# Optimization experiments

Measured on AMD Instinct MI355X. Metric: run time of the kernel, lower is better.

The kernel has to match this reference:

```python
import jax, jax.numpy as jnp
import numpy as np

N_HEAD = 16
ROPE_THETA = 10000.0


def rope_cos_sin(head_dim, T):
    # theta_i = 1 / ROPE_THETA**(2i/d), freqs = outer(positions, theta)
    inv_freq = 1.0 / (ROPE_THETA ** (np.arange(0, head_dim, 2, dtype=np.float32) / head_dim))
    pos = np.arange(T, dtype=np.float32)
    freqs = np.outer(pos, inv_freq)  # [T, d/2]
    return jnp.asarray(np.cos(freqs)), jnp.asarray(np.sin(freqs))


def apply_rope(x, cos, sin):
    # x: [B, T, H, d]; pairs are consecutive lanes (..., d/2, 2) like view_as_complex
    B, T, H, d = x.shape
    xp = x.reshape(B, T, H, d // 2, 2)
    x0, x1 = xp[..., 0], xp[..., 1]
    c = cos[None, :, None, :]  # [1, T, 1, d/2]
    s = sin[None, :, None, :]
    r0 = x0 * c - x1 * s
    r1 = x0 * s + x1 * c
    return jnp.stack([r0, r1], axis=-1).reshape(B, T, H, d)


def setup_inputs() -> dict:
    key = jax.random.key(0)
    k1, k2, k3 = jax.random.split(key, 3)
    B, T, C = 2, 2048, 1024
    x = jax.random.normal(k1, (B, T, C), dtype=jnp.float32)
    w_qkv = jax.random.normal(k2, (C, 3 * C), dtype=jnp.float32) * (1.0 / np.sqrt(C))
    w_proj = jax.random.normal(k3, (C, C), dtype=jnp.float32) * (1.0 / np.sqrt(C))
    b_proj = jnp.zeros((C,), dtype=jnp.float32)
    return {"x": x, "w_qkv": w_qkv, "w_proj": w_proj, "b_proj": b_proj}


def reference(x, w_qkv, w_proj, b_proj):
    B, T, C = x.shape
    H = N_HEAD
    d = C // H
    qkv = x @ w_qkv  # [B, T, 3C]
    q, k, v = jnp.split(qkv, 3, axis=-1)
    q = q.reshape(B, T, H, d)
    k = k.reshape(B, T, H, d)
    v = v.reshape(B, T, H, d)
    cos, sin = rope_cos_sin(d, T)
    q = apply_rope(q, cos, sin)
    k = apply_rope(k, cos, sin)
    # causal SDPA
    scale = 1.0 / np.sqrt(d).astype(np.float32)
    scores = jnp.einsum('bqhd,bkhd->bhqk', q, k) * scale  # [B, H, T, T]
    causal = jnp.tril(jnp.ones((T, T), dtype=bool))
    scores = jnp.where(causal[None, None], scores, jnp.finfo(scores.dtype).min)
    attn = jax.nn.softmax(scores, axis=-1)
    y = jnp.einsum('bhqk,bkhd->bqhd', attn, v).reshape(B, T, C)
    return y @ w_proj + b_proj
```

## Files before the change

kernel.cpp:

```cpp
#include <hip/hip_runtime.h>
#include <hip/hip_bf16.h>
#include <math.h>

typedef __bf16 bf16x8 __attribute__((ext_vector_type(8)));
typedef float floatx4 __attribute__((ext_vector_type(4)));

#define BM 128
#define BN 128

__device__ __forceinline__ void load_lds16(const void* g, void* l) {
    __builtin_amdgcn_global_load_lds(
        (const __attribute__((address_space(1))) void*)g,
        (__attribute__((address_space(3))) void*)l, 16, 0, 0);
}

__global__ __launch_bounds__(256)
void cvt_bf16_kernel(const float* __restrict__ in, __hip_bfloat16* __restrict__ out, int n8)
{
    int i = (blockIdx.x * 256 + threadIdx.x);
    if (i >= n8) return;
    const float4 a = *reinterpret_cast<const float4*>(in + (size_t)i * 8);
    const float4 b = *reinterpret_cast<const float4*>(in + (size_t)i * 8 + 4);
    union { __hip_bfloat162 h[4]; uint4 u; } pk;
    pk.h[0] = __float22bfloat162_rn(make_float2(a.x, a.y));
    pk.h[1] = __float22bfloat162_rn(make_float2(a.z, a.w));
    pk.h[2] = __float22bfloat162_rn(make_float2(b.x, b.y));
    pk.h[3] = __float22bfloat162_rn(make_float2(b.z, b.w));
    *reinterpret_cast<uint4*>(out + (size_t)i * 8) = pk.u;
}

__global__ __launch_bounds__(256)
void transpose_cvt_kernel(const float* __restrict__ in, __hip_bfloat16* __restrict__ out,
                          int R, int C)
{
    __shared__ float Ts[64][68];
    const int c0 = blockIdx.x * 64;
    const int r0 = blockIdx.y * 64;
    const int t  = threadIdx.x;
    const int lr = t >> 2;
    const int lc = (t & 3) * 16;
    #pragma unroll
    for (int j = 0; j < 16; j += 4) {
        float4 v = *reinterpret_cast<const float4*>(in + (size_t)(r0 + lr) * C + c0 + lc + j);
        Ts[lr][lc + j + 0] = v.x;
        Ts[lr][lc + j + 1] = v.y;
        Ts[lr][lc + j + 2] = v.z;
        Ts[lr][lc + j + 3] = v.w;
    }
    __syncthreads();
    const int oc = t >> 2;
    const int rs = (t & 3) * 16;
    __hip_bfloat16 tmp[16];
    #pragma unroll
    for (int j = 0; j < 16; ++j)
        tmp[j] = __float2bfloat16(Ts[rs + j][oc]);
    __hip_bfloat16* op = out + (size_t)(c0 + oc) * R + r0 + rs;
    *reinterpret_cast<uint4*>(op)     = *reinterpret_cast<uint4*>(tmp);
    *reinterpret_cast<uint4*>(op + 8) = *reinterpret_cast<uint4*>(tmp + 8);
}

template<int EPI, int CONV, int BKT, int M, int N, int K>
__global__ __launch_bounds__(256)
void gemm_kernel(const void* __restrict__ Avoid,
                 const void* __restrict__ Bvoid,
                 const float* __restrict__ bias,
                 __hip_bfloat16* __restrict__ Qo,
                 __hip_bfloat16* __restrict__ Ko,
                 __hip_bfloat16* __restrict__ Vt,
                 float* __restrict__ Out)
{
    constexpr int LD = (CONV == 0) ? BKT : 40;
    __shared__ __align__(16) __hip_bfloat16 As[BM][LD];
    __shared__ __align__(16) __hip_bfloat16 Bs[BN][LD];

    const int t    = threadIdx.x;
    const int m0   = blockIdx.y * BM;
    const int n0   = blockIdx.x * BN;
    const int lane = t & 63;
    const int w    = t >> 6;
    const int wm   = (w >> 1) * 64;
    const int wn   = (w & 1) * 64;
    const int quad = lane >> 4;
    const int l16  = lane & 15;

    floatx4 acc[4][4] = {};

    if (CONV == 0 && BKT == 32) {
        const __hip_bfloat16* A  = (const __hip_bfloat16*)Avoid;
        const __hip_bfloat16* Bt = (const __hip_bfloat16*)Bvoid;
        const int r16 = lane >> 2;
        const int gor = (lane & 3) ^ ((lane >> 3) & 3);
        const int sg  = (quad ^ ((l16 >> 1) & 3)) * 8;

        for (int k0 = 0; k0 < K; k0 += 32) {
            #pragma unroll
            for (int i = 0; i < 2; ++i) {
                int c   = 2 * w + i;
                int row = c * 16 + r16;
                load_lds16(A  + (size_t)(m0 + row) * K + k0 + gor * 8, &As[c * 16][0]);
                load_lds16(Bt + (size_t)(n0 + row) * K + k0 + gor * 8, &Bs[c * 16][0]);
            }
            __syncthreads();
            bf16x8 af[4], bfr[4];
            #pragma unroll
            for (int mf = 0; mf < 4; ++mf)
                af[mf] = *reinterpret_cast<const bf16x8*>(&As[wm + mf * 16 + l16][sg]);
            #pragma unroll
            for (int nf = 0; nf < 4; ++nf)
                bfr[nf] = *reinterpret_cast<const bf16x8*>(&Bs[wn + nf * 16 + l16][sg]);
            #pragma unroll
            for (int mf = 0; mf < 4; ++mf)
                #pragma unroll
                for (int nf = 0; nf < 4; ++nf)
                    acc[mf][nf] = __builtin_amdgcn_mfma_f32_16x16x32_bf16(
                        af[mf], bfr[nf], acc[mf][nf], 0, 0, 0);
            __syncthreads();
        }
    } else if (CONV == 0) {
        const __hip_bfloat16* A  = (const __hip_bfloat16*)Avoid;
        const __hip_bfloat16* Bt = (const __hip_bfloat16*)Bvoid;
        const int drow = lane >> 3;
        const int gsrc = (lane & 7) ^ drow;
        const int xk   = l16 & 7;

        for (int k0 = 0; k0 < K; k0 += 64) {
            #pragma unroll
            for (int i = 0; i < 4; ++i) {
                int c   = 4 * w + i;
                int row = c * 8 + drow;
                load_lds16(A  + (size_t)(m0 + row) * K + k0 + gsrc * 8, &As[c * 8][0]);
                load_lds16(Bt + (size_t)(n0 + row) * K + k0 + gsrc * 8, &Bs[c * 8][0]);
            }
            __syncthreads();
            #pragma unroll
            for (int kb = 0; kb < 2; ++kb) {
                bf16x8 af[4], bfr[4];
                #pragma unroll
                for (int mf = 0; mf < 4; ++mf)
                    af[mf] = *reinterpret_cast<const bf16x8*>(
                        &As[wm + mf * 16 + l16][((kb * 4 + quad) ^ xk) * 8]);
                #pragma unroll
                for (int nf = 0; nf < 4; ++nf)
                    bfr[nf] = *reinterpret_cast<const bf16x8*>(
                        &Bs[wn + nf * 16 + l16][((kb * 4 + quad) ^ xk) * 8]);
                #pragma unroll
                for (int mf = 0; mf < 4; ++mf)
                    #pragma unroll
                    for (int nf = 0; nf < 4; ++nf)
                        acc[mf][nf] = __builtin_amdgcn_mfma_f32_16x16x32_bf16(
                            af[mf], bfr[nf], acc[mf][nf], 0, 0, 0);
            }
            __syncthreads();
        }
    } else {
        const int sg = quad * 8;
        for (int k0 = 0; k0 < K; k0 += 32) {
            if (EPI == 0) {
                const float* A = (const float*)Avoid;
                #pragma unroll
                for (int i = 0; i < 4; ++i) {
                    int slot = t + i * 256;
                    int row  = slot >> 3;
                    int c4   = (slot & 7) << 2;
                    float4 v = *reinterpret_cast<const float4*>(A + (size_t)(m0 + row) * K + k0 + c4);
                    union { __hip_bfloat162 h2[2]; uint2 u; } pk;
                    pk.h2[0] = __float22bfloat162_rn(make_float2(v.x, v.y));
                    pk.h2[1] = __float22bfloat162_rn(make_float2(v.z, v.w));
                    *reinterpret_cast<uint2*>(&As[row][c4]) = pk.u;
                }
            } else {
                const __hip_bfloat16* A = (const __hip_bfloat16*)Avoid;
                #pragma unroll
                for (int i = 0; i < 2; ++i) {
                    int idx = t + i * 256;
                    int row = idx >> 2;
                    int col = (idx & 3) << 3;
                    *reinterpret_cast<uint4*>(&As[row][col]) =
                        *reinterpret_cast<const uint4*>(A + (size_t)(m0 + row) * K + k0 + col);
                }
            }
            const float* B = (const float*)Bvoid;
            const int bn  = t & 127;
            const int bkh = (t >> 7) * 16;
            float f[16];
            #pragma unroll
            for (int j = 0; j < 16; ++j)
                f[j] = B[(size_t)(k0 + bkh + j) * N + n0 + bn];
            #pragma unroll
            for (int c = 0; c < 4; ++c) {
                union { __hip_bfloat162 h2[2]; uint2 u; } pk;
                pk.h2[0] = __float22bfloat162_rn(make_float2(f[4*c + 0], f[4*c + 1]));
                pk.h2[1] = __float22bfloat162_rn(make_float2(f[4*c + 2], f[4*c + 3]));
                *reinterpret_cast<uint2*>(&Bs[bn][bkh + 4*c]) = pk.u;
            }
            __syncthreads();

            bf16x8 af[4], bfr[4];
            #pragma unroll
            for (int mf = 0; mf < 4; ++mf)
                af[mf] = *reinterpret_cast<const bf16x8*>(&As[wm + mf * 16 + l16][sg]);
            #pragma unroll
            for (int nf = 0; nf < 4; ++nf)
                bfr[nf] = *reinterpret_cast<const bf16x8*>(&Bs[wn + nf * 16 + l16][sg]);
            #pragma unroll
            for (int mf = 0; mf < 4; ++mf)
                #pragma unroll
                for (int nf = 0; nf < 4; ++nf)
                    acc[mf][nf] = __builtin_amdgcn_mfma_f32_16x16x32_bf16(
                        af[mf], bfr[nf], acc[mf][nf], 0, 0, 0);
            __syncthreads();
        }
    }

    if (EPI == 0) {
        #pragma unroll
        for (int mf = 0; mf < 4; ++mf) {
            #pragma unroll
            for (int nf = 0; nf < 4; ++nf) {
                #pragma unroll
                for (int r = 0; r < 4; ++r) {
                    float v = acc[mf][nf][r];
                    int m  = m0 + wm + mf * 16 + quad * 4 + r;
                    int n  = n0 + wn + nf * 16 + l16;
                    int bb = m >> 11;
                    int tp = m & 2047;
                    int which = n >> 10;
                    int dd = n & 63;
                    int h  = (n & 1023) >> 6;
                    float other = __shfl_xor(v, 1);
                    if (which < 2) {
                        int f = dd >> 1;
                        float inv = exp2f((float)f * -0.4152410118609203f);
                        float ang = (float)tp * inv;
                        float s, c;
                        __sincosf(ang, &s, &c);
                        v = (dd & 1) ? (other * s + v * c) : (v * c - other * s);
                        if (which == 0) v *= 0.1803368801111137f;
                    }
                    __hip_bfloat16 bv = __float2bfloat16(v);
                    size_t bh = (size_t)bb * 16 + h;
                    if (which == 0)      Qo[(bh * 2048 + tp) * 64 + dd] = bv;
                    else if (which == 1) Ko[(bh * 2048 + tp) * 64 + dd] = bv;
                    else                 Vt[(bh * 64 + dd) * 2048 + tp] = bv;
                }
            }
        }
    } else {
        #pragma unroll
        for (int mf = 0; mf < 4; ++mf)
            #pragma unroll
            for (int nf = 0; nf < 4; ++nf)
                #pragma unroll
                for (int r = 0; r < 4; ++r) {
                    int m = m0 + wm + mf * 16 + quad * 4 + r;
                    int n = n0 + wn + nf * 16 + l16;
                    Out[(size_t)m * N + n] = acc[mf][nf][r] + bias[n];
                }
    }
}

__global__ __launch_bounds__(256)
void attn_kernel(const __hip_bfloat16* __restrict__ Q,
                 const __hip_bfloat16* __restrict__ Kb,
                 const __hip_bfloat16* __restrict__ Vt,
                 __hip_bfloat16* __restrict__ Y)
{
    const int bh = blockIdx.x;
    const int qt = 31 - (int)blockIdx.y;
    const int bb = bh >> 4;
    const int h  = bh & 15;
    const int t    = threadIdx.x;
    const int w    = t >> 6;
    const int lane = t & 63;
    const int quad = lane >> 4;
    const int l16  = lane & 15;
    const int T = 2048;

    __shared__ __align__(16) __hip_bfloat16 Ks[64][72];
    __shared__ __align__(16) __hip_bfloat16 Vs[64][72];
    __shared__ __align__(16) __hip_bfloat16 Pl[4][16][72];

    const __hip_bfloat16* Qp = Q  + (size_t)bh * T * 64;
    const __hip_bfloat16* Kp = Kb + (size_t)bh * T * 64;
    const __hip_bfloat16* Vp = Vt + (size_t)bh * 64 * T;

    const int qrow0 = qt * 64 + w * 16;

    bf16x8 qa[2];
    #pragma unroll
    for (int kb = 0; kb < 2; ++kb)
        qa[kb] = *reinterpret_cast<const bf16x8*>(
            Qp + (size_t)(qrow0 + l16) * 64 + kb * 32 + quad * 8);

    bf16x8 ones;
    #pragma unroll
    for (int j = 0; j < 8; ++j) ones[j] = (__bf16)1.0f;

    floatx4 o[4] = {};
    floatx4 sums = {};

    const int srow = t >> 2;
    const int sch  = t & 3;
    const int ntiles = qt + 1;

    bf16x8 kreg[2], vreg[2];
    {
        const __hip_bfloat16* kg = Kp + (size_t)srow * 64 + sch * 8;
        kreg[0] = *reinterpret_cast<const bf16x8*>(kg);
        kreg[1] = *reinterpret_cast<const bf16x8*>(kg + 32);
        const __hip_bfloat16* vg = Vp + (size_t)srow * T + sch * 8;
        vreg[0] = *reinterpret_cast<const bf16x8*>(vg);
        vreg[1] = *reinterpret_cast<const bf16x8*>(vg + 32);
    }

    for (int kt = 0; kt < ntiles; ++kt) {
        __syncthreads();
        *reinterpret_cast<bf16x8*>(&Ks[srow][sch * 8])      = kreg[0];
        *reinterpret_cast<bf16x8*>(&Ks[srow][sch * 8 + 32]) = kreg[1];
        *reinterpret_cast<bf16x8*>(&Vs[srow][sch * 8])      = vreg[0];
        *reinterpret_cast<bf16x8*>(&Vs[srow][sch * 8 + 32]) = vreg[1];
        __syncthreads();
        if (kt + 1 < ntiles) {
            const __hip_bfloat16* kg = Kp + (size_t)((kt + 1) * 64 + srow) * 64 + sch * 8;
            kreg[0] = *reinterpret_cast<const bf16x8*>(kg);
            kreg[1] = *reinterpret_cast<const bf16x8*>(kg + 32);
            const __hip_bfloat16* vg = Vp + (size_t)srow * T + (kt + 1) * 64 + sch * 8;
            vreg[0] = *reinterpret_cast<const bf16x8*>(vg);
            vreg[1] = *reinterpret_cast<const bf16x8*>(vg + 32);
        }

        floatx4 sfr[4];
        #pragma unroll
        for (int nf = 0; nf < 4; ++nf) {
            floatx4 s = {};
            #pragma unroll
            for (int kb = 0; kb < 2; ++kb) {
                bf16x8 kf = *reinterpret_cast<const bf16x8*>(&Ks[nf * 16 + l16][kb * 32 + quad * 8]);
                s = __builtin_amdgcn_mfma_f32_16x16x32_bf16(qa[kb], kf, s, 0, 0, 0);
            }
            sfr[nf] = s;
        }
        if (kt == qt) {
            #pragma unroll
            for (int nf = 0; nf < 4; ++nf)
                #pragma unroll
                for (int r = 0; r < 4; ++r) {
                    int qg = w * 16 + quad * 4 + r;
                    int kg = nf * 16 + l16;
                    if (kg > qg) sfr[nf][r] = -INFINITY;
                }
        }
        #pragma unroll
        for (int nf = 0; nf < 4; ++nf)
            #pragma unroll
            for (int r = 0; r < 4; ++r)
                Pl[w][quad * 4 + r][nf * 16 + l16] = __float2bfloat16(exp2f(sfr[nf][r]));
        bf16x8 pa[2];
        #pragma unroll
        for (int kb = 0; kb < 2; ++kb)
            pa[kb] = *reinterpret_cast<const bf16x8*>(&Pl[w][l16][kb * 32 + quad * 8]);

        sums = __builtin_amdgcn_mfma_f32_16x16x32_bf16(pa[0], ones, sums, 0, 0, 0);
        sums = __builtin_amdgcn_mfma_f32_16x16x32_bf16(pa[1], ones, sums, 0, 0, 0);

        #pragma unroll
        for (int nf = 0; nf < 4; ++nf) {
            #pragma unroll
            for (int kb = 0; kb < 2; ++kb) {
                bf16x8 vb = *reinterpret_cast<const bf16x8*>(&Vs[nf * 16 + l16][kb * 32 + quad * 8]);
                o[nf] = __builtin_amdgcn_mfma_f32_16x16x32_bf16(pa[kb], vb, o[nf], 0, 0, 0);
            }
        }
    }

    #pragma unroll
    for (int r = 0; r < 4; ++r) {
        float inv = 1.0f / sums[r];
        #pragma unroll
        for (int nf = 0; nf < 4; ++nf) {
            float v = o[nf][r] * inv;
            int qrow = qrow0 + quad * 4 + r;
            int dd = nf * 16 + l16;
            Y[((size_t)bb * 2048 + qrow) * 1024 + h * 64 + dd] = __float2bfloat16(v);
        }
    }
}

extern "C" void kernel_launch(void* const* d_in, const int* in_sizes, int n_in,
                              void* d_out, int out_size, void* d_ws, size_t ws_size,
                              hipStream_t stream) {
    const float* x      = (const float*)d_in[0];
    const float* w_qkv  = (const float*)d_in[1];
    const float* w_proj = (const float*)d_in[2];
    const float* b_proj = (const float*)d_in[3];
    float* out = (float*)d_out;

    const size_t NELT = (size_t)4096 * 1024;
    const size_t WQKV = (size_t)3072 * 1024;
    const size_t WPRJ = (size_t)1024 * 1024;
    const size_t need_main = (4 * NELT + WQKV + WPRJ) * 2;
    const size_t need_fb   = 3 * NELT * 2;

    dim3 blk(256);

    if (ws_size >= need_main) {
        __hip_bfloat16* Q      = (__hip_bfloat16*)d_ws;
        __hip_bfloat16* Kb     = Q   + NELT;
        __hip_bfloat16* Vt     = Kb  + NELT;
        __hip_bfloat16* xb     = Vt  + NELT;
        __hip_bfloat16* wqkvT  = xb  + NELT;
        __hip_bfloat16* wprjT  = wqkvT + WQKV;

        cvt_bf16_kernel<<<dim3((NELT / 8 + 255) / 256), blk, 0, stream>>>(x, xb, NELT / 8);
        transpose_cvt_kernel<<<dim3(3072 / 64, 1024 / 64), blk, 0, stream>>>(w_qkv, wqkvT, 1024, 3072);
        transpose_cvt_kernel<<<dim3(1024 / 64, 1024 / 64), blk, 0, stream>>>(w_proj, wprjT, 1024, 1024);

        gemm_kernel<0, 0, 32, 4096, 3072, 1024><<<dim3(24, 32), blk, 0, stream>>>(
            xb, wqkvT, nullptr, Q, Kb, Vt, nullptr);
        attn_kernel<<<dim3(32, 32), blk, 0, stream>>>(Q, Kb, Vt, xb);
        gemm_kernel<1, 0, 64, 4096, 1024, 1024><<<dim3(8, 32), blk, 0, stream>>>(
            xb, wprjT, b_proj, nullptr, nullptr, nullptr, out);
    } else if (ws_size >= need_fb) {
        __hip_bfloat16* Q  = (__hip_bfloat16*)d_ws;
        __hip_bfloat16* Kb = Q  + NELT;
        __hip_bfloat16* Vt = Kb + NELT;

        gemm_kernel<0, 1, 32, 4096, 3072, 1024><<<dim3(24, 32), blk, 0, stream>>>(
            x, w_qkv, nullptr, Q, Kb, Vt, nullptr);
        attn_kernel<<<dim3(32, 32), blk, 0, stream>>>(Q, Kb, Vt, (__hip_bfloat16*)d_out);
        hipMemcpyAsync(Q, d_out, NELT * sizeof(__hip_bfloat16), hipMemcpyDeviceToDevice, stream);
        gemm_kernel<1, 1, 32, 4096, 1024, 1024><<<dim3(8, 32), blk, 0, stream>>>(
            Q, w_proj, b_proj, nullptr, nullptr, nullptr, out);
    } else {
        hipMemsetAsync(d_out, 0x44, (size_t)out_size * sizeof(float), stream);
    }
}
```

Before: 216.1 us.

## Merge prep kernels into one launch and add smaller-tile projection GEMM

The separate x→bf16 conversion kernel and the two weight transpose-convert kernels become a single prep kernel that dispatches on block index, removing two launches. The output projection GEMM moves from a 128x128-tile generic kernel with 256 blocks to a dedicated 128x64-tile kernel with 512 blocks, to fill more compute units on the 1024-wide output. The smaller tile lowers per-block data reuse and adds more loads of A.

```diff
diff --git a/kernel.cpp b/kernel.cpp
--- a/kernel.cpp
+++ b/kernel.cpp
@@ -14,29 +14,11 @@
         (__attribute__((address_space(3))) void*)l, 16, 0, 0);
 }
 
-__global__ __launch_bounds__(256)
-void cvt_bf16_kernel(const float* __restrict__ in, __hip_bfloat16* __restrict__ out, int n8)
-{
-    int i = (blockIdx.x * 256 + threadIdx.x);
-    if (i >= n8) return;
-    const float4 a = *reinterpret_cast<const float4*>(in + (size_t)i * 8);
-    const float4 b = *reinterpret_cast<const float4*>(in + (size_t)i * 8 + 4);
-    union { __hip_bfloat162 h[4]; uint4 u; } pk;
-    pk.h[0] = __float22bfloat162_rn(make_float2(a.x, a.y));
-    pk.h[1] = __float22bfloat162_rn(make_float2(a.z, a.w));
-    pk.h[2] = __float22bfloat162_rn(make_float2(b.x, b.y));
-    pk.h[3] = __float22bfloat162_rn(make_float2(b.z, b.w));
-    *reinterpret_cast<uint4*>(out + (size_t)i * 8) = pk.u;
-}
-
-__global__ __launch_bounds__(256)
-void transpose_cvt_kernel(const float* __restrict__ in, __hip_bfloat16* __restrict__ out,
-                          int R, int C)
+__device__ __forceinline__
+void transpose_tile(const float* __restrict__ in, __hip_bfloat16* __restrict__ out,
+                    int R, int C, int c0, int r0, int t)
 {
     __shared__ float Ts[64][68];
-    const int c0 = blockIdx.x * 64;
-    const int r0 = blockIdx.y * 64;
-    const int t  = threadIdx.x;
     const int lr = t >> 2;
     const int lc = (t & 3) * 16;
     #pragma unroll
@@ -59,7 +41,33 @@
     *reinterpret_cast<uint4*>(op + 8) = *reinterpret_cast<uint4*>(tmp + 8);
 }
 
-template<int EPI, int CONV, int BKT, int M, int N, int K>
+__global__ __launch_bounds__(256)
+void prep_kernel(const float* __restrict__ x,      __hip_bfloat16* __restrict__ xb,
+                 const float* __restrict__ w_qkv,  __hip_bfloat16* __restrict__ wqkvT,
+                 const float* __restrict__ w_proj, __hip_bfloat16* __restrict__ wprjT)
+{
+    const int bid = blockIdx.x;
+    const int t   = threadIdx.x;
+    if (bid < 2048) {
+        size_t i = (size_t)bid * 256 + t;
+        const float4 a = *reinterpret_cast<const float4*>(x + i * 8);
+        const float4 b = *reinterpret_cast<const float4*>(x + i * 8 + 4);
+        union { __hip_bfloat162 h[4]; uint4 u; } pk;
+        pk.h[0] = __float22bfloat162_rn(make_float2(a.x, a.y));
+        pk.h[1] = __float22bfloat162_rn(make_float2(a.z, a.w));
+        pk.h[2] = __float22bfloat162_rn(make_float2(b.x, b.y));
+        pk.h[3] = __float22bfloat162_rn(make_float2(b.z, b.w));
+        *reinterpret_cast<uint4*>(xb + i * 8) = pk.u;
+    } else if (bid < 2816) {
+        int q = bid - 2048;
+        transpose_tile(w_qkv, wqkvT, 1024, 3072, (q % 48) * 64, (q / 48) * 64, t);
+    } else {
+        int q = bid - 2816;
+        transpose_tile(w_proj, wprjT, 1024, 1024, (q % 16) * 64, (q / 16) * 64, t);
+    }
+}
+
+template<int EPI, int CONV, int M, int N, int K>
 __global__ __launch_bounds__(256)
 void gemm_kernel(const void* __restrict__ Avoid,
                  const void* __restrict__ Bvoid,
@@ -69,7 +77,7 @@
                  __hip_bfloat16* __restrict__ Vt,
                  float* __restrict__ Out)
 {
-    constexpr int LD = (CONV == 0) ? BKT : 40;
+    constexpr int LD = (CONV == 0) ? 32 : 40;
     __shared__ __align__(16) __hip_bfloat16 As[BM][LD];
     __shared__ __align__(16) __hip_bfloat16 Bs[BN][LD];
 
@@ -85,7 +93,7 @@
 
     floatx4 acc[4][4] = {};
 
-    if (CONV == 0 && BKT == 32) {
+    if (CONV == 0) {
         const __hip_bfloat16* A  = (const __hip_bfloat16*)Avoid;
         const __hip_bfloat16* Bt = (const __hip_bfloat16*)Bvoid;
         const int r16 = lane >> 2;
@@ -114,42 +122,6 @@
                 for (int nf = 0; nf < 4; ++nf)
                     acc[mf][nf] = __builtin_amdgcn_mfma_f32_16x16x32_bf16(
                         af[mf], bfr[nf], acc[mf][nf], 0, 0, 0);
-            __syncthreads();
-        }
-    } else if (CONV == 0) {
-        const __hip_bfloat16* A  = (const __hip_bfloat16*)Avoid;
-        const __hip_bfloat16* Bt = (const __hip_bfloat16*)Bvoid;
-        const int drow = lane >> 3;
-        const int gsrc = (lane & 7) ^ drow;
-        const int xk   = l16 & 7;
-
-        for (int k0 = 0; k0 < K; k0 += 64) {
-            #pragma unroll
-            for (int i = 0; i < 4; ++i) {
-                int c   = 4 * w + i;
-                int row = c * 8 + drow;
-                load_lds16(A  + (size_t)(m0 + row) * K + k0 + gsrc * 8, &As[c * 8][0]);
-                load_lds16(Bt + (size_t)(n0 + row) * K + k0 + gsrc * 8, &Bs[c * 8][0]);
-            }
-            __syncthreads();
-            #pragma unroll
-            for (int kb = 0; kb < 2; ++kb) {
-                bf16x8 af[4], bfr[4];
-                #pragma unroll
-                for (int mf = 0; mf < 4; ++mf)
-                    af[mf] = *reinterpret_cast<const bf16x8*>(
-                        &As[wm + mf * 16 + l16][((kb * 4 + quad) ^ xk) * 8]);
-                #pragma unroll
-                for (int nf = 0; nf < 4; ++nf)
-                    bfr[nf] = *reinterpret_cast<const bf16x8*>(
-                        &Bs[wn + nf * 16 + l16][((kb * 4 + quad) ^ xk) * 8]);
-                #pragma unroll
-                for (int mf = 0; mf < 4; ++mf)
-                    #pragma unroll
-                    for (int nf = 0; nf < 4; ++nf)
-                        acc[mf][nf] = __builtin_amdgcn_mfma_f32_16x16x32_bf16(
-                            af[mf], bfr[nf], acc[mf][nf], 0, 0, 0);
-            }
             __syncthreads();
         }
     } else {
@@ -260,6 +232,77 @@
 }
 
 __global__ __launch_bounds__(256)
+void proj_kernel(const __hip_bfloat16* __restrict__ A,
+                 const __hip_bfloat16* __restrict__ Bt,
+                 const float* __restrict__ bias,
+                 float* __restrict__ Out)
+{
+    constexpr int K = 1024, N = 1024;
+    __shared__ __align__(16) __hip_bfloat16 As[128][64];
+    __shared__ __align__(16) __hip_bfloat16 Bs[64][64];
+
+    const int t    = threadIdx.x;
+    const int m0   = blockIdx.y * 128;
+    const int n0   = blockIdx.x * 64;
+    const int lane = t & 63;
+    const int w    = t >> 6;
+    const int wm   = w * 32;
+    const int quad = lane >> 4;
+    const int l16  = lane & 15;
+
+    const int drow = lane >> 3;
+    const int gsrc = (lane & 7) ^ drow;
+    const int xk   = l16 & 7;
+
+    floatx4 acc[2][4] = {};
+
+    for (int k0 = 0; k0 < K; k0 += 64) {
+        #pragma unroll
+        for (int i = 0; i < 4; ++i) {
+            int c   = 4 * w + i;
+            int row = c * 8 + drow;
+            load_lds16(A + (size_t)(m0 + row) * K + k0 + gsrc * 8, &As[c * 8][0]);
+        }
+        #pragma unroll
+        for (int i = 0; i < 2; ++i) {
+            int c   = 2 * w + i;
+            int row = c * 8 + drow;
+            load_lds16(Bt + (size_t)(n0 + row) * K + k0 + gsrc * 8, &Bs[c * 8][0]);
+        }
+        __syncthreads();
+        #pragma unroll
+        for (int kb = 0; kb < 2; ++kb) {
+            const int slot = ((kb * 4 + quad) ^ xk) * 8;
+            bf16x8 af[2], bfr[4];
+            #pragma unroll
+            for (int mf = 0; mf < 2; ++mf)
+                af[mf] = *reinterpret_cast<const bf16x8*>(&As[wm + mf * 16 + l16][slot]);
+            #pragma unroll
+            for (int nf = 0; nf < 4; ++nf)
+                bfr[nf] = *reinterpret_cast<const bf16x8*>(&Bs[nf * 16 + l16][slot]);
+            #pragma unroll
+            for (int mf = 0; mf < 2; ++mf)
+                #pragma unroll
+                for (int nf = 0; nf < 4; ++nf)
+                    acc[mf][nf] = __builtin_amdgcn_mfma_f32_16x16x32_bf16(
+                        af[mf], bfr[nf], acc[mf][nf], 0, 0, 0);
+        }
+        __syncthreads();
+    }
+
+    #pragma unroll
+    for (int mf = 0; mf < 2; ++mf)
+        #pragma unroll
+        for (int nf = 0; nf < 4; ++nf)
+            #pragma unroll
+            for (int r = 0; r < 4; ++r) {
+                int m = m0 + wm + mf * 16 + quad * 4 + r;
+                int n = n0 + nf * 16 + l16;
+                Out[(size_t)m * N + n] = acc[mf][nf][r] + bias[n];
+            }
+}
+
+__global__ __launch_bounds__(256)
 void attn_kernel(const __hip_bfloat16* __restrict__ Q,
                  const __hip_bfloat16* __restrict__ Kb,
                  const __hip_bfloat16* __restrict__ Vt,
@@ -411,25 +454,22 @@
         __hip_bfloat16* wqkvT  = xb  + NELT;
         __hip_bfloat16* wprjT  = wqkvT + WQKV;
 
-        cvt_bf16_kernel<<<dim3((NELT / 8 + 255) / 256), blk, 0, stream>>>(x, xb, NELT / 8);
-        transpose_cvt_kernel<<<dim3(3072 / 64, 1024 / 64), blk, 0, stream>>>(w_qkv, wqkvT, 1024, 3072);
-        transpose_cvt_kernel<<<dim3(1024 / 64, 1024 / 64), blk, 0, stream>>>(w_proj, wprjT, 1024, 1024);
-
-        gemm_kernel<0, 0, 32, 4096, 3072, 1024><<<dim3(24, 32), blk, 0, stream>>>(
+        prep_kernel<<<dim3(3072), blk, 0, stream>>>(x, xb, w_qkv, wqkvT, w_proj, wprjT);
+
+        gemm_kernel<0, 0, 4096, 3072, 1024><<<dim3(24, 32), blk, 0, stream>>>(
             xb, wqkvT, nullptr, Q, Kb, Vt, nullptr);
         attn_kernel<<<dim3(32, 32), blk, 0, stream>>>(Q, Kb, Vt, xb);
-        gemm_kernel<1, 0, 64, 4096, 1024, 1024><<<dim3(8, 32), blk, 0, stream>>>(
-            xb, wprjT, b_proj, nullptr, nullptr, nullptr, out);
+        proj_kernel<<<dim3(16, 32), blk, 0, stream>>>(xb, wprjT, b_proj, out);
     } else if (ws_size >= need_fb) {
         __hip_bfloat16* Q  = (__hip_bfloat16*)d_ws;
         __hip_bfloat16* Kb = Q  + NELT;
         __hip_bfloat16* Vt = Kb + NELT;
 
-        gemm_kernel<0, 1, 32, 4096, 3072, 1024><<<dim3(24, 32), blk, 0, stream>>>(
+        gemm_kernel<0, 1, 4096, 3072, 1024><<<dim3(24, 32), blk, 0, stream>>>(
             x, w_qkv, nullptr, Q, Kb, Vt, nullptr);
         attn_kernel<<<dim3(32, 32), blk, 0, stream>>>(Q, Kb, Vt, (__hip_bfloat16*)d_out);
         hipMemcpyAsync(Q, d_out, NELT * sizeof(__hip_bfloat16), hipMemcpyDeviceToDevice, stream);
-        gemm_kernel<1, 1, 32, 4096, 1024, 1024><<<dim3(8, 32), blk, 0, stream>>>(
+        gemm_kernel<1, 1, 4096, 1024, 1024><<<dim3(8, 32), blk, 0, stream>>>(
             Q, w_proj, b_proj, nullptr, nullptr, nullptr, out);
     } else {
         hipMemsetAsync(d_out, 0x44, (size_t)out_size * sizeof(float), stream);
```

Measured after the change: 208.0 us. 1.04x faster.
